# Optimization experiments

Hardware: AMD Instinct MI355X
Metric: run time of the kernel (lower is better)

## Reference

```python
import jax, jax.numpy as jnp
import numpy as np

# Module hyperparameters (from __init__ defaults)
P, Q = 16, 12          # pool_output_size
KH, KW = 3, 3          # kernel_size
SH, SW = 2, 2          # stride
PH, PW = 1, 1          # padding
THRESH = 0.05
GATE_SCALE = 10.0
C_IN = 3
OUT_FEATURES = 512


def setup_inputs() -> dict:
    key = jax.random.key(0)
    k1, k2 = jax.random.split(key)
    x = jax.random.normal(k1, (64, C_IN, 512, 384), dtype=jnp.float32)
    flat = C_IN * P * Q  # 576
    proj_weight = jax.random.normal(k2, (flat, OUT_FEATURES), dtype=jnp.float32) * (1.0 / flat ** 0.5)
    proj_bias = jnp.zeros((OUT_FEATURES,), dtype=jnp.float32)
    return {"x": x, "proj_weight": proj_weight, "proj_bias": proj_bias}


def reference(x, proj_weight, proj_bias):
    N, C, H, W = x.shape
    # 1. AdaptiveAvgPool2d to (P,Q): H,W chosen divisible -> uniform average pooling
    pooled = x.reshape(N, C, P, H // P, Q, W // Q).mean(axis=(3, 5))  # (N,C,P,Q)
    # 2. Threshold: keep x where x > THRESH else 0
    thr = jnp.where(pooled > THRESH, pooled, 0.0)
    # 3. Unfold into overlapping patches (N, C*KH*KW, L)
    pad = jnp.pad(thr, ((0, 0), (0, 0), (PH, PH), (PW, PW)))
    OH = (P + 2 * PH - KH) // SH + 1  # 8
    OW = (Q + 2 * PW - KW) // SW + 1  # 6
    rows = (jnp.arange(OH) * SH)[:, None] + jnp.arange(KH)[None, :]  # (OH,KH)
    cols = (jnp.arange(OW) * SW)[:, None] + jnp.arange(KW)[None, :]  # (OW,KW)
    patch6 = pad[:, :, rows[:, :, None, None], cols[None, None, :, :]]  # (N,C,OH,KH,OW,KW)
    patches = patch6.transpose(0, 1, 3, 5, 2, 4).reshape(N, C * KH * KW, OH * OW)  # (N,C*9,L)
    # 4. Per-patch mean -> sigmoid gate, 5. scale and fold (scatter-add) back
    gate = jax.nn.sigmoid(patches.mean(axis=1, keepdims=True) * GATE_SCALE)  # (N,1,L)
    gated = patches * gate
    g6 = gated.reshape(N, C, KH, KW, OH, OW).transpose(0, 1, 4, 2, 5, 3)  # (N,C,OH,KH,OW,KW)
    folded = jnp.zeros((N, C, P + 2 * PH, Q + 2 * PW), dtype=x.dtype)
    folded = folded.at[:, :, rows[:, :, None, None], cols[None, None, :, :]].add(g6)
    folded = folded[:, :, PH:PH + P, PW:PW + Q]  # (N,C,P,Q)
    # 6. Flatten and project
    return folded.reshape(N, -1) @ proj_weight + proj_bias
```

## Files before the change

kernel.cpp:

```cpp
#include <hip/hip_runtime.h>
#include <math.h>

#define NB   64
#define CIN  3
#define PP   16
#define QQ   12

typedef float f32x4 __attribute__((ext_vector_type(4)));

__global__ __launch_bounds__(256)
void pool_kernel(const float* __restrict__ x, float* __restrict__ pooled)
{
    const int t  = threadIdx.x;
    const int o  = blockIdx.x * 4 + (t >> 6);
    const int l  = t & 63;
    const int strip = o / QQ;
    const int q     = o - strip * QQ;

    const f32x4* base = reinterpret_cast<const f32x4*>(x) + (size_t)strip * 3072
                      + q * 8 + (l & 7);
    const int r0 = l >> 3;

    f32x4 v0 = base[(r0 +  0) * 96];
    f32x4 v1 = base[(r0 +  8) * 96];
    f32x4 v2 = base[(r0 + 16) * 96];
    f32x4 v3 = base[(r0 + 24) * 96];

    float s = ((v0.x + v0.y) + (v0.z + v0.w))
            + ((v1.x + v1.y) + (v1.z + v1.w))
            + ((v2.x + v2.y) + (v2.z + v2.w))
            + ((v3.x + v3.y) + (v3.z + v3.w));

#pragma unroll
    for (int off = 32; off >= 1; off >>= 1)
        s += __shfl_xor(s, off, 64);

    if (l == 0)
        pooled[o] = s * (1.0f / 1024.0f);
}

__global__ __launch_bounds__(512)
void head_kernel(const float* __restrict__ pooled,
                 const float* __restrict__ Wt,
                 const float* __restrict__ bias,
                 float* __restrict__ out)
{
    const int blk = blockIdx.x;
    const int n   = blk >> 3;
    const int jc  = blk & 7;
    const int t   = threadIdx.x;
    const int l   = t & 63;
    const int kc  = t >> 6;

    __shared__ float thr[576];
    __shared__ float gate[48];
    __shared__ float f[576];
    __shared__ float part[512];

    for (int k = t; k < 576; k += 512) {
        float p = pooled[n * 576 + k];
        thr[k] = (p > 0.05f) ? p : 0.f;
    }
    __syncthreads();

    if (t < 48) {
        int oh = t / 6, ow = t - oh * 6;
        float S = 0.f;
#pragma unroll
        for (int c = 0; c < 3; ++c)
#pragma unroll
            for (int kh = 0; kh < 3; ++kh)
#pragma unroll
                for (int kw = 0; kw < 3; ++kw) {
                    int r  = oh * 2 + kh - 1;
                    int sx = ow * 2 + kw - 1;
                    if (r >= 0 && r < PP && sx >= 0 && sx < QQ)
                        S += thr[c * 192 + r * 12 + sx];
                }
        gate[t] = 1.f / (1.f + expf(-S * (10.0f / 27.0f)));
    }
    __syncthreads();

    for (int k = t; k < 576; k += 512) {
        int ij = k % 192;
        int i = ij / 12, j = ij - i * 12;
        int r = i + 1, sx = j + 1;
        float g = 0.f;
#pragma unroll
        for (int kh = 0; kh < 3; ++kh) {
            int oh2 = r - kh;
            if (oh2 < 0 || (oh2 & 1) || (oh2 >> 1) >= 8) continue;
            int oh = oh2 >> 1;
#pragma unroll
            for (int kw = 0; kw < 3; ++kw) {
                int ow2 = sx - kw;
                if (ow2 < 0 || (ow2 & 1) || (ow2 >> 1) >= 6) continue;
                g += gate[oh * 6 + (ow2 >> 1)];
            }
        }
        f[k] = thr[k] * g;
    }
    __syncthreads();

    const int j  = jc * 64 + l;
    const int k0 = kc * 72;
    const float* Wp = Wt + (size_t)k0 * 512 + j;
    float a0 = 0.f, a1 = 0.f, a2 = 0.f, a3 = 0.f;
#pragma unroll 6
    for (int kk = 0; kk < 72; kk += 4) {
        a0 = fmaf(f[k0 + kk + 0], Wp[(size_t)(kk + 0) * 512], a0);
        a1 = fmaf(f[k0 + kk + 1], Wp[(size_t)(kk + 1) * 512], a1);
        a2 = fmaf(f[k0 + kk + 2], Wp[(size_t)(kk + 2) * 512], a2);
        a3 = fmaf(f[k0 + kk + 3], Wp[(size_t)(kk + 3) * 512], a3);
    }
    part[t] = (a0 + a1) + (a2 + a3);
    __syncthreads();

    if (t < 64) {
        float acc = bias[j];
#pragma unroll
        for (int c = 0; c < 8; ++c)
            acc += part[c * 64 + t];
        out[n * 512 + j] = acc;
    }
}

extern "C" void kernel_launch(void* const* d_in, const int* in_sizes, int n_in,
                              void* d_out, int out_size, void* d_ws, size_t ws_size,
                              hipStream_t stream)
{
    const float* x    = (const float*)d_in[0];
    const float* Wt   = (const float*)d_in[1];
    const float* bias = (const float*)d_in[2];
    float* out = (float*)d_out;
    float* pooled = (float*)d_ws;

    pool_kernel<<<(NB * CIN * PP * QQ) / 4, 256, 0, stream>>>(x, pooled);
    head_kernel<<<NB * 8, 512, 0, stream>>>(pooled, Wt, bias, out);
}
```

Baseline: 33.79 us.

## Batch eight samples per head block to reuse projection weight loads

The head kernel now handles eight samples per block instead of one, so each weight value loaded from global memory is applied to eight feature vectors held in shared memory. This cuts total weight traffic eightfold and shrinks the grid from 512 to 64 blocks. The per-sample threshold, gate and fold stages are spread across all threads. The partial-sum buffer reuses the threshold array's shared memory. The trade-off is far fewer blocks in flight on a many-CU GPU, more shared memory and registers per block, and a head stage that is likely small next to the bandwidth-bound pooling pass.

```diff
diff --git a/kernel.cpp b/kernel.cpp
--- a/kernel.cpp
+++ b/kernel.cpp
@@ -45,26 +45,26 @@
                  const float* __restrict__ bias,
                  float* __restrict__ out)
 {
-    const int blk = blockIdx.x;
-    const int n   = blk >> 3;
-    const int jc  = blk & 7;
-    const int t   = threadIdx.x;
-    const int l   = t & 63;
-    const int kc  = t >> 6;
+    const int sg = blockIdx.x >> 3;
+    const int jc = blockIdx.x & 7;
+    const int t  = threadIdx.x;
+    const int l  = t & 63;
+    const int kc = t >> 6;
 
-    __shared__ float thr[576];
-    __shared__ float gate[48];
-    __shared__ float f[576];
-    __shared__ float part[512];
+    __shared__ float thr[8][576];
+    __shared__ float gate[8][48];
+    __shared__ float f[8][576];
 
-    for (int k = t; k < 576; k += 512) {
-        float p = pooled[n * 576 + k];
-        thr[k] = (p > 0.05f) ? p : 0.f;
+    for (int k = t; k < 8 * 576; k += 512) {
+        int s = k / 576, kk = k - s * 576;
+        float p = pooled[(sg * 8 + s) * 576 + kk];
+        thr[s][kk] = (p > 0.05f) ? p : 0.f;
     }
     __syncthreads();
 
-    if (t < 48) {
-        int oh = t / 6, ow = t - oh * 6;
+    if (t < 384) {
+        int s = t / 48, g = t - s * 48;
+        int oh = g / 6, ow = g - oh * 6;
         float S = 0.f;
 #pragma unroll
         for (int c = 0; c < 3; ++c)
@@ -75,14 +75,15 @@
                     int r  = oh * 2 + kh - 1;
                     int sx = ow * 2 + kw - 1;
                     if (r >= 0 && r < PP && sx >= 0 && sx < QQ)
-                        S += thr[c * 192 + r * 12 + sx];
+                        S += thr[s][c * 192 + r * 12 + sx];
                 }
-        gate[t] = 1.f / (1.f + expf(-S * (10.0f / 27.0f)));
+        gate[s][g] = 1.f / (1.f + expf(-S * (10.0f / 27.0f)));
     }
     __syncthreads();
 
-    for (int k = t; k < 576; k += 512) {
-        int ij = k % 192;
+    for (int k = t; k < 8 * 576; k += 512) {
+        int s = k / 576, kk = k - s * 576;
+        int ij = kk % 192;
         int i = ij / 12, j = ij - i * 12;
         int r = i + 1, sx = j + 1;
         float g = 0.f;
@@ -95,10 +96,10 @@
             for (int kw = 0; kw < 3; ++kw) {
                 int ow2 = sx - kw;
                 if (ow2 < 0 || (ow2 & 1) || (ow2 >> 1) >= 6) continue;
-                g += gate[oh * 6 + (ow2 >> 1)];
+                g += gate[s][oh * 6 + (ow2 >> 1)];
             }
         }
-        f[k] = thr[k] * g;
+        f[s][kk] = thr[s][kk] * g;
     }
     __syncthreads();
 
@@ -106,22 +107,45 @@
     const int k0 = kc * 72;
     const float* Wp = Wt + (size_t)k0 * 512 + j;
     float a0 = 0.f, a1 = 0.f, a2 = 0.f, a3 = 0.f;
-#pragma unroll 6
+    float a4 = 0.f, a5 = 0.f, a6 = 0.f, a7 = 0.f;
+#pragma unroll 3
     for (int kk = 0; kk < 72; kk += 4) {
-        a0 = fmaf(f[k0 + kk + 0], Wp[(size_t)(kk + 0) * 512], a0);
-        a1 = fmaf(f[k0 + kk + 1], Wp[(size_t)(kk + 1) * 512], a1);
-        a2 = fmaf(f[k0 + kk + 2], Wp[(size_t)(kk + 2) * 512], a2);
-        a3 = fmaf(f[k0 + kk + 3], Wp[(size_t)(kk + 3) * 512], a3);
+        const float w0 = Wp[(size_t)(kk + 0) * 512];
+        const float w1 = Wp[(size_t)(kk + 1) * 512];
+        const float w2 = Wp[(size_t)(kk + 2) * 512];
+        const float w3 = Wp[(size_t)(kk + 3) * 512];
+#define HEAD_FMA(S, ACC)                                                   \
+        {                                                                  \
+            const f32x4 fv = *reinterpret_cast<const f32x4*>(&f[S][k0 + kk]); \
+            ACC = fmaf(fv.x, w0, ACC);                                     \
+            ACC = fmaf(fv.y, w1, ACC);                                     \
+            ACC = fmaf(fv.z, w2, ACC);                                     \
+            ACC = fmaf(fv.w, w3, ACC);                                     \
+        }
+        HEAD_FMA(0, a0) HEAD_FMA(1, a1) HEAD_FMA(2, a2) HEAD_FMA(3, a3)
+        HEAD_FMA(4, a4) HEAD_FMA(5, a5) HEAD_FMA(6, a6) HEAD_FMA(7, a7)
+#undef HEAD_FMA
     }
-    part[t] = (a0 + a1) + (a2 + a3);
+
+    float* part = &thr[0][0];
+    part[0 * 512 + kc * 64 + l] = a0;
+    part[1 * 512 + kc * 64 + l] = a1;
+    part[2 * 512 + kc * 64 + l] = a2;
+    part[3 * 512 + kc * 64 + l] = a3;
+    part[4 * 512 + kc * 64 + l] = a4;
+    part[5 * 512 + kc * 64 + l] = a5;
+    part[6 * 512 + kc * 64 + l] = a6;
+    part[7 * 512 + kc * 64 + l] = a7;
     __syncthreads();
 
-    if (t < 64) {
-        float acc = bias[j];
+    {
+        const int s2 = t >> 6;
+        const int l2 = t & 63;
+        float a = bias[jc * 64 + l2];
 #pragma unroll
         for (int c = 0; c < 8; ++c)
-            acc += part[c * 64 + t];
-        out[n * 512 + j] = acc;
+            a += part[s2 * 512 + c * 64 + l2];
+        out[(sg * 8 + s2) * 512 + jc * 64 + l2] = a;
     }
 }
 
@@ -136,5 +160,5 @@
     float* pooled = (float*)d_ws;
 
     pool_kernel<<<(NB * CIN * PP * QQ) / 4, 256, 0, stream>>>(x, pooled);
-    head_kernel<<<NB * 8, 512, 0, stream>>>(pooled, Wt, bias, out);
+    head_kernel<<<64, 512, 0, stream>>>(pooled, Wt, bias, out);
 }
```

After: 42.87 us. 1.27x slower.
